# Kernel optimization log

Measured on AMD Instinct MI355X. Metric: run time of the kernel, lower is better.

## Reference

```python
import jax, jax.numpy as jnp
import numpy as np

T, B, D_IN, D_LAT, D_OUT = 2048, 64, 256, 256, 256


def _linear_params(key, fan_in, fan_out):
    kw, kb = jax.random.split(key)
    bound = 1.0 / np.sqrt(fan_in)
    W = jax.random.uniform(kw, (fan_out, fan_in), jnp.float32, -bound, bound)
    b = jax.random.uniform(kb, (fan_out,), jnp.float32, -bound, bound)
    return W, b


def setup_inputs() -> dict:
    key = jax.random.key(0)
    ks = jax.random.split(key, 6)
    Wf, bf = _linear_params(ks[0], D_IN + D_LAT, D_LAT)
    Wi, bi = _linear_params(ks[1], D_IN + D_LAT, D_LAT)
    Wo, bo = _linear_params(ks[2], D_IN + D_LAT, D_LAT)
    Wc, bc = _linear_params(ks[3], D_IN + D_LAT, D_LAT)
    Wout, bout = _linear_params(ks[4], D_LAT, D_OUT)
    x = jax.random.normal(ks[5], (T, B, D_IN), jnp.float32)
    h0 = jnp.zeros((B, D_LAT), jnp.float32)
    C0 = jnp.zeros((B, D_LAT), jnp.float32)
    return {"x": x, "h0": h0, "C0": C0,
            "Wf": Wf, "bf": bf, "Wi": Wi, "bi": bi,
            "Wo": Wo, "bo": bo, "Wc": Wc, "bc": bc,
            "Wout": Wout, "bout": bout}


def reference(x, h0, C0, Wf, bf, Wi, bi, Wo, bo, Wc, bc, Wout, bout):
    def step(carry, x_t):
        h, C = carry
        comb = jnp.concatenate([x_t, h], axis=-1)  # [B, D_IN+D_LAT]
        f_t = jax.nn.sigmoid(comb @ Wf.T + bf)
        i_t = jax.nn.sigmoid(comb @ Wi.T + bi)
        o_t = jax.nn.sigmoid(comb @ Wo.T + bo)
        C_tilde = jnp.tanh(comb @ Wc.T + bc)
        C_new = f_t * C + i_t * C_tilde
        h_new = o_t * jnp.tanh(C_new)
        out = h_new @ Wout.T + bout
        return (h_new, C_new), (out, h_new)
    (h_f, C_f), (outputs, hidden_states) = jax.lax.scan(step, (h0, C0), x)
    return outputs, hidden_states, C_f
```

## Files before the change

kernel.cpp:

```cpp
#include <hip/hip_runtime.h>
#include <cstdint>
#include <cstddef>

#define T_STEPS 2048
#define BATCH 64

typedef _Float16 f16;
typedef _Float16 f16x2 __attribute__((ext_vector_type(2)));
typedef _Float16 f16x8 __attribute__((ext_vector_type(8)));
typedef float f32x4 __attribute__((ext_vector_type(4)));
typedef unsigned int uint32;
typedef uint32 u32x4 __attribute__((ext_vector_type(4)));

__device__ __forceinline__ float dot2(uint32 w, uint32 h, float c) {
  f16x2 a = __builtin_bit_cast(f16x2, w);
  f16x2 b = __builtin_bit_cast(f16x2, h);
  return __builtin_amdgcn_fdot2(a, b, c, false);
}

__device__ __forceinline__ float dot8(u32x4 w, u32x4 h, float c) {
  c = dot2(w[0], h[0], c);
  c = dot2(w[1], h[1], c);
  c = dot2(w[2], h[2], c);
  c = dot2(w[3], h[3], c);
  return c;
}

__device__ __forceinline__ uint32 pack2(f16 a, f16 b) {
  f16x2 t; t[0] = a; t[1] = b;
  return __builtin_bit_cast(uint32, t);
}

__device__ __forceinline__ u32x4 packrow(const float* p) {
  u32x4 v;
  #pragma unroll
  for (int kk = 0; kk < 4; ++kk) {
    const float2 f = *(const float2*)(p + kk * 2);
    v[kk] = pack2((f16)f.x, (f16)f.y);
  }
  return v;
}

__global__ __launch_bounds__(256) void setup_weights(
    const float* __restrict__ Wf, const float* __restrict__ Wi,
    const float* __restrict__ Wo, const float* __restrict__ Wc,
    const float* __restrict__ Wout,
    f16* __restrict__ wx16, f16* __restrict__ wout16)
{
  int id = blockIdx.x * 256 + threadIdx.x;
  const float* WG_[4] = {Wf, Wi, Wo, Wc};
  if (id < 262144) {
    int n = id >> 8, k = id & 255;
    int G = n >> 8, j = n & 255;
    wx16[id] = (f16)WG_[G][j * 512 + k];
    return;
  }
  id -= 262144;
  if (id < 65536) { wout16[id] = (f16)Wout[id]; return; }
}

__global__ __launch_bounds__(256) void setup_state(
    const float* __restrict__ h0, const float* __restrict__ C0,
    f16* __restrict__ hstate, float* __restrict__ c32)
{
  int id = blockIdx.x * 256 + threadIdx.x;
  if (id < 16384) { hstate[id] = (f16)h0[id]; return; }
  id -= 16384;
  if (id < 16384) c32[id] = C0[id];
}

template<int A_F32, int OUT_F32_BIAS>
__global__ __launch_bounds__(256) void gemm_k(
    const void* __restrict__ Av, const f16* __restrict__ B,
    void* __restrict__ Cv, const float* __restrict__ bias, int N)
{
  constexpr int LDA = 264;
  __shared__ f16 As[128 * 264];
  __shared__ f16 Bs[128 * 264];
  const int tid = threadIdx.x;
  const int m0 = blockIdx.x * 128;
  const int n0 = blockIdx.y * 128;

  if (A_F32) {
    const float* A = (const float*)Av;
    #pragma unroll
    for (int j = 0; j < 32; ++j) {
      int flat = (tid + j * 256) * 4;
      int row = flat >> 8, col = flat & 255;
      const float4 v = *(const float4*)(A + (size_t)(m0 + row) * 256 + col);
      uint2 u; u.x = pack2((f16)v.x, (f16)v.y); u.y = pack2((f16)v.z, (f16)v.w);
      *(uint2*)&As[row * LDA + col] = u;
    }
  } else {
    const f16* A = (const f16*)Av;
    #pragma unroll
    for (int j = 0; j < 32; ++j) {
      int flat = (tid + j * 256) * 4;
      int row = flat >> 8, col = flat & 255;
      *(uint2*)&As[row * LDA + col] = *(const uint2*)(A + (size_t)(m0 + row) * 256 + col);
    }
  }
  #pragma unroll
  for (int j = 0; j < 32; ++j) {
    int flat = (tid + j * 256) * 4;
    int row = flat >> 8, col = flat & 255;
    *(uint2*)&Bs[row * LDA + col] = *(const uint2*)(B + (size_t)(n0 + row) * 256 + col);
  }
  __syncthreads();

  const int wave = tid >> 6, l = tid & 63;
  const int wr = wave >> 1, wc = wave & 1;
  const int lr = l & 15, lq = l >> 4;

  f32x4 acc[4][4] = {};
  #pragma unroll
  for (int kk = 0; kk < 8; ++kk) {
    f16x8 a[4], b[4];
    #pragma unroll
    for (int mi = 0; mi < 4; ++mi)
      a[mi] = *(const f16x8*)&As[(64 * wr + 16 * mi + lr) * LDA + kk * 32 + lq * 8];
    #pragma unroll
    for (int ni = 0; ni < 4; ++ni)
      b[ni] = *(const f16x8*)&Bs[(64 * wc + 16 * ni + lr) * LDA + kk * 32 + lq * 8];
    #pragma unroll
    for (int mi = 0; mi < 4; ++mi)
      #pragma unroll
      for (int ni = 0; ni < 4; ++ni)
        acc[mi][ni] = __builtin_amdgcn_mfma_f32_16x16x32_f16(a[mi], b[ni], acc[mi][ni], 0, 0, 0);
  }

  #pragma unroll
  for (int mi = 0; mi < 4; ++mi) {
    #pragma unroll
    for (int ni = 0; ni < 4; ++ni) {
      int col = n0 + 64 * wc + 16 * ni + lr;
      float bv = 0.f;
      if (OUT_F32_BIAS) bv = bias[col];
      #pragma unroll
      for (int v = 0; v < 4; ++v) {
        int row = m0 + 64 * wr + 16 * mi + lq * 4 + v;
        if (OUT_F32_BIAS) ((float*)Cv)[(size_t)row * N + col] = acc[mi][ni][v] + bv;
        else              ((f16*)Cv)[(size_t)row * N + col] = (f16)acc[mi][ni][v];
      }
    }
  }
}

#define RL25(M) M(0) M(1) M(2) M(3) M(4) M(5) M(6) M(7) M(8) M(9) M(10) M(11) \
  M(12) M(13) M(14) M(15) M(16) M(17) M(18) M(19) M(20) M(21) M(22) M(23) M(24)
#define RL7(M) M(0) M(1) M(2) M(3) M(4) M(5) M(6)

__global__ __launch_bounds__(1024) void lstm_persist(
    const float* __restrict__ Wf, const float* __restrict__ Wi,
    const float* __restrict__ Wo, const float* __restrict__ Wc,
    const float* __restrict__ bf, const float* __restrict__ bi,
    const float* __restrict__ bo, const float* __restrict__ bc,
    const f16* __restrict__ xproj, f16* __restrict__ hstate,
    float* __restrict__ c32, float* __restrict__ hid_out,
    f16* __restrict__ h16c, float* __restrict__ cf_out, int t0, int Tc)
{
  __shared__ u32x4 wtail[7 * 1024];
  __shared__ uint32 h_lds[128] __attribute__((aligned(16)));
  __shared__ float part[4 * 260];

  const int tid = threadIdx.x;
  const int r = blockIdx.x;
  const int G = tid >> 8, jj = tid & 255;

  const float* WGp = (G == 0) ? Wf : (G == 1) ? Wi : (G == 2) ? Wo : Wc;
  const float* bGp = (G == 0) ? bf : (G == 1) ? bi : (G == 2) ? bo : bc;
  const float* row = WGp + (size_t)jj * 512 + 256;

#define DECLW(i) u32x4 w##i;
  RL25(DECLW)
#undef DECLW
#define LOADW(i) w##i = packrow(row + (i) * 8);
  RL25(LOADW)
#undef LOADW
#define TSTORE(i) wtail[(i) * 1024 + tid] = packrow(row + 200 + (i) * 8);
  RL7(TSTORE)
#undef TSTORE

  const float biasv = bGp[jj];

  float Creg = 0.f;
  if (tid < 256) Creg = c32[r * 256 + tid];
  if (tid < 128) h_lds[tid] = ((const uint32*)hstate)[r * 128 + tid];
  __syncthreads();

  for (int tl = 0; tl < Tc; ++tl) {
    const int gt = t0 + tl;

    const float xpv = (float)xproj[((size_t)tl * 64 + r) * 1024 + (G << 8) + jj];

    int otid;
    asm volatile("v_mov_b32 %0, %1" : "=v"(otid) : "v"(tid));

    float acc = 0.f;
#define DOTW(i) { const u32x4 hh = *(const u32x4*)&h_lds[(i) * 4]; \
                  acc = dot8(w##i, hh, acc); }
    RL25(DOTW)
#undef DOTW
#define TDOT(i) { const u32x4 hh = *(const u32x4*)&h_lds[(25 + (i)) * 4]; \
                  const u32x4 tw = wtail[(i) * 1024 + otid]; \
                  acc = dot8(tw, hh, acc); }
    RL7(TDOT)
#undef TDOT

    part[G * 260 + jj] = acc + xpv + biasv;
    __syncthreads();

    if (tid < 256) {
      const float pf = part[tid];
      const float pi = part[260 + tid];
      const float po = part[520 + tid];
      const float pc = part[780 + tid];
      const float f_ = __builtin_amdgcn_rcpf(1.f + __expf(-pf));
      const float i_ = __builtin_amdgcn_rcpf(1.f + __expf(-pi));
      const float o_ = __builtin_amdgcn_rcpf(1.f + __expf(-po));
      const float cb = 1.f - 2.f * __builtin_amdgcn_rcpf(__expf(2.f * pc) + 1.f);
      const float Cn = f_ * Creg + i_ * cb;
      Creg = Cn;
      const float th = 1.f - 2.f * __builtin_amdgcn_rcpf(__expf(2.f * Cn) + 1.f);
      const float hn = o_ * th;
      hid_out[((size_t)gt * 64 + r) * 256 + tid] = hn;
      const f16 h16v = (f16)hn;
      ((unsigned short*)h_lds)[tid] = __builtin_bit_cast(unsigned short, h16v);
      h16c[((size_t)tl * 64 + r) * 256 + tid] = h16v;
      if (gt == T_STEPS - 1) cf_out[r * 256 + tid] = Cn;
    }
    __syncthreads();
  }

  if (tid < 256) c32[r * 256 + tid] = Creg;
  if (tid < 128) ((uint32*)hstate)[r * 128 + tid] = h_lds[tid];
}

extern "C" void kernel_launch(void* const* d_in, const int* in_sizes, int n_in,
                              void* d_out, int out_size, void* d_ws, size_t ws_size,
                              hipStream_t stream)
{
  const float* x    = (const float*)d_in[0];
  const float* h0   = (const float*)d_in[1];
  const float* C0   = (const float*)d_in[2];
  const float* Wf   = (const float*)d_in[3];
  const float* bf   = (const float*)d_in[4];
  const float* Wi   = (const float*)d_in[5];
  const float* bi   = (const float*)d_in[6];
  const float* Wo   = (const float*)d_in[7];
  const float* bo   = (const float*)d_in[8];
  const float* Wc   = (const float*)d_in[9];
  const float* bc   = (const float*)d_in[10];
  const float* Wout = (const float*)d_in[11];
  const float* bout = (const float*)d_in[12];
  float* out = (float*)d_out;

  char* w = (char*)d_ws;
  f16*    wx16   = (f16*)w;    w += (size_t)1024 * 256 * 2;
  f16*    wout16 = (f16*)w;    w += (size_t)256 * 256 * 2;
  f16*    hstate = (f16*)w;    w += (size_t)64 * 256 * 2;
  float*  c32    = (float*)w;  w += (size_t)64 * 256 * 4;
  const size_t fixedB = (size_t)(w - (char*)d_ws);

  int Tc = 2;
  const int cands[] = {2048, 1024, 512, 256, 128, 64, 32, 16, 8, 4, 2};
  for (int c : cands) {
    if (fixedB + (size_t)c * 163840 <= ws_size) { Tc = c; break; }
  }

  f16* xproj = (f16*)w;
  f16* h16c  = (f16*)(w + (size_t)Tc * 64 * 1024 * 2);

  setup_weights<<<1280, 256, 0, stream>>>(Wf, Wi, Wo, Wc, Wout, wx16, wout16);
  setup_state<<<128, 256, 0, stream>>>(h0, C0, hstate, c32);

  float* hid_out = out + (size_t)T_STEPS * 64 * 256;
  float* cf_out  = out + (size_t)2 * T_STEPS * 64 * 256;

  for (int t0 = 0; t0 < T_STEPS; t0 += Tc) {
    gemm_k<1, 0><<<dim3(Tc * 64 / 128, 8), 256, 0, stream>>>(
        x + (size_t)t0 * 64 * 256, wx16, xproj, nullptr, 1024);
    lstm_persist<<<64, 1024, 0, stream>>>(Wf, Wi, Wo, Wc, bf, bi, bo, bc,
                                          xproj, hstate, c32,
                                          hid_out, h16c, cf_out, t0, Tc);
    gemm_k<0, 1><<<dim3(Tc * 64 / 128, 2), 256, 0, stream>>>(
        h16c, wout16, out + (size_t)t0 * 64 * 256, bout, 256);
  }
}
```

Before: 4.154 ms.

## Stream recurrent weights from prepacked global buffer, shrink register-held slice

```diff
diff --git a/kernel.cpp b/kernel.cpp
--- a/kernel.cpp
+++ b/kernel.cpp
@@ -31,21 +31,11 @@
   return __builtin_bit_cast(uint32, t);
 }
 
-__device__ __forceinline__ u32x4 packrow(const float* p) {
-  u32x4 v;
-  #pragma unroll
-  for (int kk = 0; kk < 4; ++kk) {
-    const float2 f = *(const float2*)(p + kk * 2);
-    v[kk] = pack2((f16)f.x, (f16)f.y);
-  }
-  return v;
-}
-
 __global__ __launch_bounds__(256) void setup_weights(
     const float* __restrict__ Wf, const float* __restrict__ Wi,
     const float* __restrict__ Wo, const float* __restrict__ Wc,
     const float* __restrict__ Wout,
-    f16* __restrict__ wx16, f16* __restrict__ wout16)
+    f16* __restrict__ wx16, f16* __restrict__ wout16, uint32* __restrict__ whp)
 {
   int id = blockIdx.x * 256 + threadIdx.x;
   const float* WG_[4] = {Wf, Wi, Wo, Wc};
@@ -57,6 +47,14 @@
   }
   id -= 262144;
   if (id < 65536) { wout16[id] = (f16)Wout[id]; return; }
+  id -= 65536;
+  if (id < 131072) {
+    int kq = id >> 12, rem = id & 4095;
+    int o = rem >> 2, c = rem & 3;
+    int G = o >> 8, j = o & 255;
+    const float* src = WG_[G] + j * 512 + 256 + kq * 8 + c * 2;
+    whp[id] = pack2((f16)src[0], (f16)src[1]);
+  }
 }
 
 __global__ __launch_bounds__(256) void setup_state(
@@ -146,20 +144,17 @@
   }
 }
 
-#define RL25(M) M(0) M(1) M(2) M(3) M(4) M(5) M(6) M(7) M(8) M(9) M(10) M(11) \
-  M(12) M(13) M(14) M(15) M(16) M(17) M(18) M(19) M(20) M(21) M(22) M(23) M(24)
-#define RL7(M) M(0) M(1) M(2) M(3) M(4) M(5) M(6)
+#define RL8(M) M(0) M(1) M(2) M(3) M(4) M(5) M(6) M(7)
 
 __global__ __launch_bounds__(1024) void lstm_persist(
-    const float* __restrict__ Wf, const float* __restrict__ Wi,
-    const float* __restrict__ Wo, const float* __restrict__ Wc,
+    const uint32* __restrict__ whp,
     const float* __restrict__ bf, const float* __restrict__ bi,
     const float* __restrict__ bo, const float* __restrict__ bc,
     const f16* __restrict__ xproj, f16* __restrict__ hstate,
     float* __restrict__ c32, float* __restrict__ hid_out,
     f16* __restrict__ h16c, float* __restrict__ cf_out, int t0, int Tc)
 {
-  __shared__ u32x4 wtail[7 * 1024];
+  __shared__ u32x4 wtail[9 * 1024];
   __shared__ uint32 h_lds[128] __attribute__((aligned(16)));
   __shared__ float part[4 * 260];
 
@@ -167,19 +162,14 @@
   const int r = blockIdx.x;
   const int G = tid >> 8, jj = tid & 255;
 
-  const float* WGp = (G == 0) ? Wf : (G == 1) ? Wi : (G == 2) ? Wo : Wc;
   const float* bGp = (G == 0) ? bf : (G == 1) ? bi : (G == 2) ? bo : bc;
-  const float* row = WGp + (size_t)jj * 512 + 256;
-
-#define DECLW(i) u32x4 w##i;
-  RL25(DECLW)
-#undef DECLW
-#define LOADW(i) w##i = packrow(row + (i) * 8);
-  RL25(LOADW)
+  const u32x4* wq = (const u32x4*)whp;
+
+#define LOADW(i) u32x4 w##i = wq[(i) * 1024 + tid];
+  RL8(LOADW)
 #undef LOADW
-#define TSTORE(i) wtail[(i) * 1024 + tid] = packrow(row + 200 + (i) * 8);
-  RL7(TSTORE)
-#undef TSTORE
+  #pragma unroll
+  for (int i = 0; i < 9; ++i) wtail[i * 1024 + tid] = wq[(23 + i) * 1024 + tid];
 
   const float biasv = bGp[jj];
 
@@ -199,13 +189,19 @@
     float acc = 0.f;
 #define DOTW(i) { const u32x4 hh = *(const u32x4*)&h_lds[(i) * 4]; \
                   acc = dot8(w##i, hh, acc); }
-    RL25(DOTW)
+    RL8(DOTW)
 #undef DOTW
-#define TDOT(i) { const u32x4 hh = *(const u32x4*)&h_lds[(25 + (i)) * 4]; \
-                  const u32x4 tw = wtail[(i) * 1024 + otid]; \
-                  acc = dot8(tw, hh, acc); }
-    RL7(TDOT)
-#undef TDOT
+    #pragma unroll
+    for (int kq = 8; kq < 23; ++kq) {
+      const u32x4 hh = *(const u32x4*)&h_lds[kq * 4];
+      const u32x4 wv = wq[kq * 1024 + otid];
+      acc = dot8(wv, hh, acc);
+    }
+    #pragma unroll
+    for (int i = 0; i < 9; ++i) {
+      const u32x4 hh = *(const u32x4*)&h_lds[(23 + i) * 4];
+      acc = dot8(wtail[i * 1024 + otid], hh, acc);
+    }
 
     part[G * 260 + jj] = acc + xpv + biasv;
     __syncthreads();
@@ -258,6 +254,7 @@
   char* w = (char*)d_ws;
   f16*    wx16   = (f16*)w;    w += (size_t)1024 * 256 * 2;
   f16*    wout16 = (f16*)w;    w += (size_t)256 * 256 * 2;
+  uint32* whp    = (uint32*)w; w += (size_t)131072 * 4;
   f16*    hstate = (f16*)w;    w += (size_t)64 * 256 * 2;
   float*  c32    = (float*)w;  w += (size_t)64 * 256 * 4;
   const size_t fixedB = (size_t)(w - (char*)d_ws);
@@ -271,7 +268,8 @@
   f16* xproj = (f16*)w;
   f16* h16c  = (f16*)(w + (size_t)Tc * 64 * 1024 * 2);
 
-  setup_weights<<<1280, 256, 0, stream>>>(Wf, Wi, Wo, Wc, Wout, wx16, wout16);
+  setup_weights<<<1792, 256, 0, stream>>>(Wf, Wi, Wo, Wc, Wout,
+                                          wx16, wout16, whp);
   setup_state<<<128, 256, 0, stream>>>(h0, C0, hstate, c32);
 
   float* hid_out = out + (size_t)T_STEPS * 64 * 256;
@@ -280,7 +278,7 @@
   for (int t0 = 0; t0 < T_STEPS; t0 += Tc) {
     gemm_k<1, 0><<<dim3(Tc * 64 / 128, 8), 256, 0, stream>>>(
         x + (size_t)t0 * 64 * 256, wx16, xproj, nullptr, 1024);
-    lstm_persist<<<64, 1024, 0, stream>>>(Wf, Wi, Wo, Wc, bf, bi, bo, bc,
+    lstm_persist<<<64, 1024, 0, stream>>>(whp, bf, bi, bo, bc,
                                           xproj, hstate, c32,
                                           hid_out, h16c, cf_out, t0, Tc);
     gemm_k<0, 1><<<dim3(Tc * 64 / 128, 2), 256, 0, stream>>>(
```

After: 6.131 ms. 47.6% more time.
